# Performance work log

Measured on AMD Instinct MI355X. Metric: run time of the kernel, lower is better.

Reference implementation:

```python
import jax, jax.numpy as jnp
import numpy as np

B, L, D, H = 4, 1024, 1024, 16
HD = D // H            # head_dim = 64
MAX_LEN = 1024         # pos_max_len
SCALE = HD ** 0.5


def setup_inputs() -> dict:
    key = jax.random.key(0)
    ks = jax.random.split(key, 7)
    sd = 1.0 / np.sqrt(D)
    x = jax.random.normal(ks[0], (B, L, D), dtype=jnp.float32)
    Wq = jax.random.normal(ks[1], (D, D), dtype=jnp.float32) * sd
    Wk = jax.random.normal(ks[2], (D, D), dtype=jnp.float32) * sd
    Wv = jax.random.normal(ks[3], (D, D), dtype=jnp.float32) * sd
    Wo = jax.random.normal(ks[4], (D, D), dtype=jnp.float32) * sd
    # relative positional embedding tables [2*max_len+1, head_dim]
    pek = jax.random.normal(ks[5], (2 * MAX_LEN + 1, HD), dtype=jnp.float32) / np.sqrt(HD)
    pev = jax.random.normal(ks[6], (2 * MAX_LEN + 1, HD), dtype=jnp.float32) / np.sqrt(HD)
    return {"x": x, "Wq": Wq, "Wk": Wk, "Wv": Wv, "Wo": Wo, "pek": pek, "pev": pev}


def _rel_idx(seq_len):
    r = jnp.arange(seq_len)
    dist = r[None, :] - r[:, None]                 # k - q, [L, L]
    return jnp.clip(dist, -MAX_LEN, MAX_LEN) + MAX_LEN


def reference(x, Wq, Wk, Wv, Wo, pek, pev):
    b, s, _ = x.shape
    # projections (nn.Linear: x @ W.T), split heads -> [b, h, s, d]
    def proj(W):
        return (x @ W.T).reshape(b, s, H, HD).transpose(0, 2, 1, 3)
    Q, K, V = proj(Wq), proj(Wk), proj(Wv)

    scores = jnp.einsum('bhqd,bhkd->bhqk', Q, K) / SCALE
    idx = _rel_idx(s)                              # [s, s]
    rel_k = pek[idx]                               # [s, s, hd]
    scores = scores + jnp.einsum('bhqd,qkd->bhqk', Q, rel_k) / SCALE

    causal = jnp.tril(jnp.ones((s, s), dtype=bool))
    scores = jnp.where(causal[None, None], scores, -jnp.inf)
    attn = jax.nn.softmax(scores, axis=-1)         # [b, h, q, k]

    out = jnp.einsum('bhqk,bhkd->bhqd', attn, V)
    rel_v = pev[idx]                               # [s, s, hd]
    out = out + jnp.einsum('bhqk,qkd->bhqd', attn, rel_v)

    out = out.transpose(0, 2, 1, 3).reshape(b, s, D)
    return out @ Wo.T
```

## Files before the change

### kernel.cpp

```cpp
#include <hip/hip_runtime.h>
#include <hip/hip_bf16.h>

typedef __hip_bfloat16 bf16;
using bfv8 = __attribute__((ext_vector_type(8))) __bf16;
using f4_t = __attribute__((ext_vector_type(4))) float;

#define DEVI static __device__ __forceinline__

DEVI unsigned short f2bu(float f) {
    bf16 h = __float2bfloat16(f);
    return __builtin_bit_cast(unsigned short, h);
}
DEVI ushort4 f4_to_b4(float4 v) {
    ushort4 r;
    r.x = f2bu(v.x); r.y = f2bu(v.y); r.z = f2bu(v.z); r.w = f2bu(v.w);
    return r;
}
DEVI void gl2lds16(const void* g, void* l) {
    __builtin_amdgcn_global_load_lds((const __attribute__((address_space(1))) void*)g,
                                     (__attribute__((address_space(3))) void*)l, 16, 0, 0);
}

template<int N>
DEVI float row_ror(float x) {
    return __builtin_bit_cast(float,
        __builtin_amdgcn_update_dpp(0, __builtin_bit_cast(int, x), 0x120 | N, 0xF, 0xF, false));
}
DEVI float max16(float x) {
    x = fmaxf(x, row_ror<8>(x));
    x = fmaxf(x, row_ror<4>(x));
    x = fmaxf(x, row_ror<2>(x));
    x = fmaxf(x, row_ror<1>(x));
    return x;
}
DEVI float sum16(float x) {
    x += row_ror<8>(x);
    x += row_ror<4>(x);
    x += row_ror<2>(x);
    x += row_ror<1>(x);
    return x;
}

__global__ __launch_bounds__(256) void prep_cast(
    const float* __restrict__ x, const float* __restrict__ wq, const float* __restrict__ wk,
    const float* __restrict__ wv, const float* __restrict__ wo,
    bf16* __restrict__ xb, bf16* __restrict__ wqb, bf16* __restrict__ wkb,
    bf16* __restrict__ wvb, bf16* __restrict__ wob)
{
    size_t i = (size_t)blockIdx.x * 256 + threadIdx.x;
    const size_t X4 = 1u << 20, W4 = 1u << 18;
    const float* src; bf16* dst; size_t off;
    if (i < X4)              { src = x;  dst = xb;  off = i; }
    else if (i < X4 + W4)    { src = wq; dst = wqb; off = i - X4; }
    else if (i < X4 + 2*W4)  { src = wk; dst = wkb; off = i - X4 - W4; }
    else if (i < X4 + 3*W4)  { src = wv; dst = wvb; off = i - X4 - 2*W4; }
    else                     { src = wo; dst = wob; off = i - X4 - 3*W4; }
    float4 v = ((const float4*)src)[off];
    ((ushort4*)dst)[off] = f4_to_b4(v);
}

__global__ __launch_bounds__(256) void prep_blocks(
    const float* __restrict__ pek, const float* __restrict__ pev,
    bf16* __restrict__ pekBlk, bf16* __restrict__ pevBlk)
{
    __shared__ bf16 t[64][72];
    const int b = blockIdx.x;
    const int r = threadIdx.x >> 2, c0 = (threadIdx.x & 3) * 16;

    if (b < 17) {
        const float* src = pek + (size_t)(64 * b + 1 + r) * 64 + c0;
        bf16* dst = pekBlk + (size_t)b * 4096 + r * 64 + c0;
#pragma unroll
        for (int j = 0; j < 16; j += 4)
            *(ushort4*)(dst + j) = f4_to_b4(*(const float4*)(src + j));
    }
    {
        const float* src = pev + (size_t)(64 * b + 1 + r) * 64 + c0;
#pragma unroll
        for (int j = 0; j < 16; j++) t[r][c0 + j] = __float2bfloat16(src[j]);
        __syncthreads();
        bf16* dst = pevBlk + (size_t)b * 4096 + r * 64 + c0;
#pragma unroll
        for (int j = 0; j < 16; j++) dst[j] = t[c0 + j][r];
    }
}

__global__ __launch_bounds__(256) void transpose_v(const bf16* __restrict__ Vb, bf16* __restrict__ Vtb)
{
    __shared__ __align__(16) bf16 t[64][72];
    const int bh = blockIdx.y, l0 = blockIdx.x * 64;
    const int r = threadIdx.x >> 2, c0 = (threadIdx.x & 3) * 16;
    const bf16* src = Vb + ((size_t)(bh << 10) + l0 + r) * 64 + c0;
    *(int4*)&t[r][c0]     = *(const int4*)src;
    *(int4*)&t[r][c0 + 8] = *(const int4*)(src + 8);
    __syncthreads();
    int4 o[2]; bf16* ob = (bf16*)o;
#pragma unroll
    for (int j = 0; j < 16; j++) ob[j] = t[c0 + j][r];
    bf16* dst = Vtb + ((size_t)(bh << 6) + r) * 1024 + l0 + c0;
    *(int4*)dst = o[0]; *(int4*)(dst + 8) = o[1];
}

__global__ __launch_bounds__(256) void gemm_bt2(
    const bf16* __restrict__ A,
    const bf16* __restrict__ B0, const bf16* __restrict__ B1, const bf16* __restrict__ B2,
    bf16* __restrict__ outb, float* __restrict__ outf, int K, int mode)
{
    __shared__ __align__(16) bf16 As[128 * 64];
    __shared__ __align__(16) bf16 Bs[128 * 64];

    const int tid  = threadIdx.x;
    const int lane = tid & 63, wave = tid >> 6;
    const int quad = lane >> 4, l16 = lane & 15;
    const int wr = wave >> 1, wc = wave & 1;
    const int m0 = blockIdx.y * 128, n0 = blockIdx.x * 128;
    const int z = blockIdx.z;
    const bf16* Bm = (z == 0) ? B0 : (z == 1) ? B1 : B2;

    f4_t zero = {0.f, 0.f, 0.f, 0.f};
    f4_t acc[4][4];
#pragma unroll
    for (int i = 0; i < 4; i++)
#pragma unroll
        for (int j = 0; j < 4; j++) acc[i][j] = zero;

    const int srow = 32 * wave + (lane >> 3);
    const int scol = (lane & 7) * 8;
    const bf16* Ag = A  + (size_t)(m0 + srow) * K + scol;
    const bf16* Bg = Bm + (size_t)(n0 + srow) * K + scol;

    for (int k0 = 0; k0 < K; k0 += 64) {
#pragma unroll
        for (int i = 0; i < 4; i++) {
            gl2lds16(Ag + (size_t)(8 * i) * K + k0, &As[(32 * wave + 8 * i) * 64]);
            gl2lds16(Bg + (size_t)(8 * i) * K + k0, &Bs[(32 * wave + 8 * i) * 64]);
        }
        __syncthreads();
#pragma unroll
        for (int ks = 0; ks < 2; ks++) {
            bfv8 af[4], bfr[4];
#pragma unroll
            for (int mt = 0; mt < 4; mt++)
                af[mt] = *(const bfv8*)&As[(wr * 64 + mt * 16 + l16) * 64 + ks * 32 + quad * 8];
#pragma unroll
            for (int nt = 0; nt < 4; nt++)
                bfr[nt] = *(const bfv8*)&Bs[(wc * 64 + nt * 16 + l16) * 64 + ks * 32 + quad * 8];
#pragma unroll
            for (int mt = 0; mt < 4; mt++)
#pragma unroll
                for (int nt = 0; nt < 4; nt++)
                    acc[mt][nt] = __builtin_amdgcn_mfma_f32_16x16x32_bf16(af[mt], bfr[nt], acc[mt][nt], 0, 0, 0);
        }
        __syncthreads();
    }

    if (mode == 0) {
        bf16* ob = outb + (size_t)z * (4 * 16 * 1024 * 64);
#pragma unroll
        for (int mt = 0; mt < 4; mt++)
#pragma unroll
            for (int nt = 0; nt < 4; nt++)
#pragma unroll
                for (int r = 0; r < 4; r++) {
                    int m = m0 + wr * 64 + mt * 16 + quad * 4 + r;
                    int n = n0 + wc * 64 + nt * 16 + l16;
                    int b = m >> 10, l = m & 1023, h = n >> 6, hd = n & 63;
                    ob[((size_t)(b * 16 + h) * 1024 + l) * 64 + hd] = __float2bfloat16(acc[mt][nt][r]);
                }
    } else {
#pragma unroll
        for (int mt = 0; mt < 4; mt++)
#pragma unroll
            for (int nt = 0; nt < 4; nt++)
#pragma unroll
                for (int r = 0; r < 4; r++) {
                    int m = m0 + wr * 64 + mt * 16 + quad * 4 + r;
                    int n = n0 + wc * 64 + nt * 16 + l16;
                    outf[(size_t)m * 1024 + n] = acc[mt][nt][r];
                }
    }
}

__global__ __launch_bounds__(256) void attn_k(
    const bf16* __restrict__ Qb, const bf16* __restrict__ Kb, const bf16* __restrict__ Vtb,
    const bf16* __restrict__ pekBlk, const bf16* __restrict__ pevBlk, bf16* __restrict__ Ob)
{
    constexpr int ST = 104;
    __shared__ __align__(16) bf16 Ks[64 * 64];
    __shared__ __align__(16) bf16 Vs[64 * 64];
    __shared__ __align__(16) bf16 pekR[2 * 4096];
    __shared__ __align__(16) bf16 pevR[3 * 4096];
    __shared__ __align__(16) bf16 sU[4][16 * ST];
    __shared__ __align__(16) bf16 sP[4][16 * 72];

    const int tid  = threadIdx.x;
    const int lane = tid & 63, wave = tid >> 6;
    const int quad = lane >> 4, l16 = lane & 15;
    const int bh = blockIdx.x;
    const int g  = 15 - blockIdx.y;
    const int s  = 4 * g + wave;
    const int nkt = g + 1;

    bf16* myU = sU[wave];
    bf16* myP = sP[wave];

    const int srow8 = lane >> 3;
    const int scg   = (lane & 7) ^ srow8;
    const int x8    = l16 & 7;

    {
        int* p = (int*)myU;
#pragma unroll
        for (int i = 0; i < 13; i++) p[lane + 64 * i] = 0;
    }

    bfv8 qf[2];
    {
        const bf16* qp = Qb + ((size_t)bh * 1024 + 16 * s + l16) * 64 + quad * 8;
        qf[0] = *(const bfv8*)qp;
        qf[1] = *(const bfv8*)(qp + 32);
#pragma unroll
        for (int j = 0; j < 8; j++) {
            qf[0][j] = (__bf16)((float)qf[0][j] * 0.125f);
            qf[1][j] = (__bf16)((float)qf[1][j] * 0.125f);
        }
    }

    f4_t zero = {0.f, 0.f, 0.f, 0.f};
    f4_t o_acc[4];
    float m_i[4], l_i[4];
#pragma unroll
    for (int i = 0; i < 4; i++) { o_acc[i] = zero; m_i[i] = -1e30f; l_i[i] = 0.f; }

    const bf16* Kbh = Kb  + (size_t)bh * 1024 * 64;
    const bf16* Vbh = Vtb + (size_t)bh * 64 * 1024;
    const int B0 = 15 - g;

#pragma unroll
    for (int i = 0; i < 2; i++) {
        const int row = 8 * wave + 32 * i + srow8;
        gl2lds16(Kbh + (size_t)row * 64 + scg * 8, &Ks[(8 * wave + 32 * i) * 64]);
        gl2lds16(Vbh + (size_t)row * 1024 + scg * 8, &Vs[(8 * wave + 32 * i) * 64]);
    }
#pragma unroll
    for (int i2 = 0; i2 < 2; i2++) {
        const int slot = (B0 + i2) & 1;
#pragma unroll
        for (int i = 0; i < 2; i++) {
            const int row = 16 * wave + 8 * i + srow8;
            gl2lds16(pekBlk + (size_t)(B0 + i2) * 4096 + row * 64 + scg * 8,
                     &pekR[slot * 4096 + (16 * wave + 8 * i) * 64]);
        }
    }
#pragma unroll
    for (int i2 = 0; i2 < 3; i2++) {
        const int slot = (B0 + i2) % 3;
#pragma unroll
        for (int i = 0; i < 2; i++) {
            const int row = 16 * wave + 8 * i + srow8;
            gl2lds16(pevBlk + (size_t)(B0 + i2) * 4096 + row * 64 + scg * 8,
                     &pevR[slot * 4096 + (16 * wave + 8 * i) * 64]);
        }
    }

    for (int kt = 0; kt < nkt; kt++) {
        const int k0 = kt << 6;
        const int Bb = kt - g + 15;
        const int bm3 = Bb % 3;

        if (kt > 0) {
#pragma unroll
            for (int i = 0; i < 2; i++) {
                const int row = 8 * wave + 32 * i + srow8;
                gl2lds16(Kbh + (size_t)(k0 + row) * 64 + scg * 8, &Ks[(8 * wave + 32 * i) * 64]);
                gl2lds16(Vbh + (size_t)row * 1024 + k0 + scg * 8, &Vs[(8 * wave + 32 * i) * 64]);
            }
            const int bNew = Bb + 1, cNew = Bb + 2;
            const int slotK = bNew & 1, slotV = cNew % 3;
#pragma unroll
            for (int i = 0; i < 2; i++) {
                const int row = 16 * wave + 8 * i + srow8;
                gl2lds16(pekBlk + (size_t)bNew * 4096 + row * 64 + scg * 8,
                         &pekR[slotK * 4096 + (16 * wave + 8 * i) * 64]);
                gl2lds16(pevBlk + (size_t)cNew * 4096 + row * 64 + scg * 8,
                         &pevR[slotV * 4096 + (16 * wave + 8 * i) * 64]);
            }
        }
        __syncthreads();

        f4_t s1[4], tt[5];
#pragma unroll
        for (int i = 0; i < 4; i++) s1[i] = zero;
#pragma unroll
        for (int i = 0; i < 5; i++) tt[i] = zero;
#pragma unroll
        for (int ks = 0; ks < 2; ks++) {
#pragma unroll
            for (int nt = 0; nt < 4; nt++) {
                bfv8 kf = *(const bfv8*)&Ks[(nt * 16 + l16) * 64 + ((ks * 4 + quad) ^ x8) * 8];
                s1[nt] = __builtin_amdgcn_mfma_f32_16x16x32_bf16(qf[ks], kf, s1[nt], 0, 0, 0);
            }
#pragma unroll
            for (int nt = 0; nt < 5; nt++) {
                const int off  = 48 - 16 * wave + 16 * nt;
                const int slot = (Bb + (off >> 6)) & 1;
                bfv8 pf = *(const bfv8*)&pekR[slot * 4096 + ((off & 63) + l16) * 64
                                              + ((ks * 4 + quad) ^ x8) * 8];
                tt[nt] = __builtin_amdgcn_mfma_f32_16x16x32_bf16(qf[ks], pf, tt[nt], 0, 0, 0);
            }
        }

        float sc[4][4];
#pragma unroll
        for (int r = 0; r < 4; r++) {
            int qq = quad * 4 + r;
            int t  = l16 + 15 - qq;
            int srcl = quad * 16 + (t & 15);
            bool lo = (t < 16);
            float rot[5];
#pragma unroll
            for (int j = 0; j < 5; j++) rot[j] = __shfl(tt[j][r], srcl, 64);
#pragma unroll
            for (int nt = 0; nt < 4; nt++) {
                float s2 = lo ? rot[nt] : rot[nt + 1];
                float v = s1[nt][r] + s2;
                int kk = nt * 16 + l16;
                if (k0 + kk > 16 * s + qq) v = -1e30f;
                sc[nt][r] = v;
            }
        }

        float alpha[4];
#pragma unroll
        for (int r = 0; r < 4; r++) {
            float mt = fmaxf(fmaxf(sc[0][r], sc[1][r]), fmaxf(sc[2][r], sc[3][r]));
            mt = max16(mt);
            float mnew = fmaxf(m_i[r], mt);
            alpha[r] = __expf(m_i[r] - mnew);
            m_i[r] = mnew;
        }
#pragma unroll
        for (int nt = 0; nt < 4; nt++)
#pragma unroll
            for (int r = 0; r < 4; r++)
                sc[nt][r] = __expf(sc[nt][r] - m_i[r]);
#pragma unroll
        for (int r = 0; r < 4; r++) {
            float rs = sum16(sc[0][r] + sc[1][r] + sc[2][r] + sc[3][r]);
            l_i[r] = l_i[r] * alpha[r] + rs;
#pragma unroll
            for (int nt = 0; nt < 4; nt++) o_acc[nt][r] *= alpha[r];
        }

#pragma unroll
        for (int nt = 0; nt < 4; nt++)
#pragma unroll
            for (int r = 0; r < 4; r++) {
                int qq = quad * 4 + r;
                int kk = nt * 16 + l16;
                bf16 pb = __float2bfloat16(sc[nt][r]);
                myP[qq * 72 + kk] = pb;
                myU[qq * ST + kk - qq + 15] = pb;
            }

#pragma unroll
        for (int ks = 0; ks < 2; ks++) {
            bfv8 pa = *(const bfv8*)&myP[l16 * 72 + ks * 32 + quad * 8];
#pragma unroll
            for (int nt = 0; nt < 4; nt++) {
                bfv8 vf = *(const bfv8*)&Vs[(nt * 16 + l16) * 64 + ((ks * 4 + quad) ^ x8) * 8];
                o_acc[nt] = __builtin_amdgcn_mfma_f32_16x16x32_bf16(pa, vf, o_acc[nt], 0, 0, 0);
            }
        }
#pragma unroll
        for (int ks = 0; ks < 3; ks++) {
            bfv8 ua = *(const bfv8*)&myU[l16 * ST + ks * 32 + quad * 8];
            const int off2 = 48 - 16 * wave + 32 * ks + 8 * quad;
            int slot2 = bm3 + (off2 >> 6);
            if (slot2 >= 3) slot2 -= 3;
            const int chunk = (((off2 & 63) >> 3) ^ x8);
#pragma unroll
            for (int nt = 0; nt < 4; nt++) {
                bfv8 pvf = *(const bfv8*)&pevR[slot2 * 4096 + (nt * 16 + l16) * 64 + chunk * 8];
                o_acc[nt] = __builtin_amdgcn_mfma_f32_16x16x32_bf16(ua, pvf, o_acc[nt], 0, 0, 0);
            }
        }
        __syncthreads();
    }

    const int b = bh >> 4, h = bh & 15;
#pragma unroll
    for (int nt = 0; nt < 4; nt++)
#pragma unroll
        for (int r = 0; r < 4; r++) {
            int q = 16 * s + quad * 4 + r;
            int d = nt * 16 + l16;
            Ob[((size_t)(b * 1024 + q)) * 1024 + h * 64 + d] = __float2bfloat16(o_acc[nt][r] / l_i[r]);
        }
}

extern "C" void kernel_launch(void* const* d_in, const int* in_sizes, int n_in,
                              void* d_out, int out_size, void* d_ws, size_t ws_size,
                              hipStream_t stream) {
    const float* x   = (const float*)d_in[0];
    const float* Wq  = (const float*)d_in[1];
    const float* Wk  = (const float*)d_in[2];
    const float* Wv  = (const float*)d_in[3];
    const float* Wo  = (const float*)d_in[4];
    const float* pek = (const float*)d_in[5];
    const float* pev = (const float*)d_in[6];

    const size_t MB = 1u << 20;
    char* ws = (char*)d_ws;
    bf16* xb     = (bf16*)(ws + 0);
    bf16* Wqb    = (bf16*)(ws + 8  * MB);
    bf16* Wkb    = (bf16*)(ws + 10 * MB);
    bf16* Wvb    = (bf16*)(ws + 12 * MB);
    bf16* Wob    = (bf16*)(ws + 14 * MB);
    bf16* Qb     = (bf16*)(ws + 16 * MB);
    bf16* Kb     = (bf16*)(ws + 24 * MB);
    bf16* Vb     = (bf16*)(ws + 32 * MB);
    bf16* Vtb    = (bf16*)(ws + 40 * MB);
    bf16* pekBlk = (bf16*)(ws + 48 * MB);
    bf16* pevBlk = (bf16*)(ws + 48 * MB + 256*1024);
    bf16* Ao     = xb;

    prep_cast<<<dim3(8192), 256, 0, stream>>>(x, Wq, Wk, Wv, Wo, xb, Wqb, Wkb, Wvb, Wob);
    prep_blocks<<<dim3(18), 256, 0, stream>>>(pek, pev, pekBlk, pevBlk);
    gemm_bt2<<<dim3(8, 32, 3), 256, 0, stream>>>(xb, Wqb, Wkb, Wvb, Qb, nullptr, 1024, 0);
    transpose_v<<<dim3(16, 64), 256, 0, stream>>>(Vb, Vtb);
    attn_k<<<dim3(64, 16), 256, 0, stream>>>(Qb, Kb, Vtb, pekBlk, pevBlk, Ao);
    gemm_bt2<<<dim3(8, 32, 1), 256, 0, stream>>>(Ao, Wob, nullptr, nullptr, nullptr, (float*)d_out, 1024, 1);
}
```

Measured before the change: 247.8 us.

## Register-prefetch next tiles in GEMM and attention, halve GEMM M-tile

Both the projection GEMM and the attention kernel now load the next K/V/pek/pev or A/B tile into registers before computing the current tile, then write it to LDS after a barrier. This hides global load latency behind MFMA work, where the old code issued async global-to-LDS loads and waited on them right away. The GEMM tile shrinks from 128x128 to 64x128 and the grid doubles, giving more blocks to fill the CUs. The cost is more registers, extra LDS store instructions, and the loss of the direct global-to-LDS path.

```diff
diff --git a/kernel.cpp b/kernel.cpp
--- a/kernel.cpp
+++ b/kernel.cpp
@@ -106,75 +106,91 @@
     const bf16* __restrict__ B0, const bf16* __restrict__ B1, const bf16* __restrict__ B2,
     bf16* __restrict__ outb, float* __restrict__ outf, int K, int mode)
 {
-    __shared__ __align__(16) bf16 As[128 * 64];
+    __shared__ __align__(16) bf16 As[64 * 64];
     __shared__ __align__(16) bf16 Bs[128 * 64];
 
     const int tid  = threadIdx.x;
     const int lane = tid & 63, wave = tid >> 6;
     const int quad = lane >> 4, l16 = lane & 15;
     const int wr = wave >> 1, wc = wave & 1;
-    const int m0 = blockIdx.y * 128, n0 = blockIdx.x * 128;
+    const int m0 = blockIdx.y * 64, n0 = blockIdx.x * 128;
     const int z = blockIdx.z;
     const bf16* Bm = (z == 0) ? B0 : (z == 1) ? B1 : B2;
 
     f4_t zero = {0.f, 0.f, 0.f, 0.f};
-    f4_t acc[4][4];
+    f4_t acc[2][4];
+#pragma unroll
+    for (int i = 0; i < 2; i++)
+#pragma unroll
+        for (int j = 0; j < 4; j++) acc[i][j] = zero;
+
+    const int srow8 = lane >> 3;
+    const int scol  = (lane & 7) * 8;
+    const bf16* Ag = A  + (size_t)(m0 + 16 * wave + srow8) * K + scol;
+    const bf16* Bg = Bm + (size_t)(n0 + 32 * wave + srow8) * K + scol;
+
+#pragma unroll
+    for (int i = 0; i < 2; i++)
+        gl2lds16(Ag + (size_t)(8 * i) * K, &As[(16 * wave + 8 * i) * 64]);
 #pragma unroll
     for (int i = 0; i < 4; i++)
-#pragma unroll
-        for (int j = 0; j < 4; j++) acc[i][j] = zero;
-
-    const int srow = 32 * wave + (lane >> 3);
-    const int scol = (lane & 7) * 8;
-    const bf16* Ag = A  + (size_t)(m0 + srow) * K + scol;
-    const bf16* Bg = Bm + (size_t)(n0 + srow) * K + scol;
-
-    for (int k0 = 0; k0 < K; k0 += 64) {
-#pragma unroll
-        for (int i = 0; i < 4; i++) {
-            gl2lds16(Ag + (size_t)(8 * i) * K + k0, &As[(32 * wave + 8 * i) * 64]);
-            gl2lds16(Bg + (size_t)(8 * i) * K + k0, &Bs[(32 * wave + 8 * i) * 64]);
-        }
+        gl2lds16(Bg + (size_t)(8 * i) * K, &Bs[(32 * wave + 8 * i) * 64]);
+
+    for (int k0 = 0;;) {
         __syncthreads();
+        const bool more = (k0 + 64 < K);
+        int4 pa[2], pb[4];
+        if (more) {
+#pragma unroll
+            for (int i = 0; i < 2; i++) pa[i] = *(const int4*)(Ag + (size_t)(8 * i) * K + k0 + 64);
+#pragma unroll
+            for (int i = 0; i < 4; i++) pb[i] = *(const int4*)(Bg + (size_t)(8 * i) * K + k0 + 64);
+        }
 #pragma unroll
         for (int ks = 0; ks < 2; ks++) {
-            bfv8 af[4], bfr[4];
-#pragma unroll
-            for (int mt = 0; mt < 4; mt++)
-                af[mt] = *(const bfv8*)&As[(wr * 64 + mt * 16 + l16) * 64 + ks * 32 + quad * 8];
+            bfv8 af[2], bfr[4];
+#pragma unroll
+            for (int mt = 0; mt < 2; mt++)
+                af[mt] = *(const bfv8*)&As[(wr * 32 + mt * 16 + l16) * 64 + ks * 32 + quad * 8];
 #pragma unroll
             for (int nt = 0; nt < 4; nt++)
                 bfr[nt] = *(const bfv8*)&Bs[(wc * 64 + nt * 16 + l16) * 64 + ks * 32 + quad * 8];
 #pragma unroll
-            for (int mt = 0; mt < 4; mt++)
+            for (int mt = 0; mt < 2; mt++)
 #pragma unroll
                 for (int nt = 0; nt < 4; nt++)
                     acc[mt][nt] = __builtin_amdgcn_mfma_f32_16x16x32_bf16(af[mt], bfr[nt], acc[mt][nt], 0, 0, 0);
         }
+        if (!more) break;
         __syncthreads();
+#pragma unroll
+        for (int i = 0; i < 2; i++) *(int4*)&As[(16 * wave + 8 * i) * 64 + lane * 8] = pa[i];
+#pragma unroll
+        for (int i = 0; i < 4; i++) *(int4*)&Bs[(32 * wave + 8 * i) * 64 + lane * 8] = pb[i];
+        k0 += 64;
     }
 
     if (mode == 0) {
         bf16* ob = outb + (size_t)z * (4 * 16 * 1024 * 64);
 #pragma unroll
-        for (int mt = 0; mt < 4; mt++)
+        for (int mt = 0; mt < 2; mt++)
 #pragma unroll
             for (int nt = 0; nt < 4; nt++)
 #pragma unroll
                 for (int r = 0; r < 4; r++) {
-                    int m = m0 + wr * 64 + mt * 16 + quad * 4 + r;
+                    int m = m0 + wr * 32 + mt * 16 + quad * 4 + r;
                     int n = n0 + wc * 64 + nt * 16 + l16;
                     int b = m >> 10, l = m & 1023, h = n >> 6, hd = n & 63;
                     ob[((size_t)(b * 16 + h) * 1024 + l) * 64 + hd] = __float2bfloat16(acc[mt][nt][r]);
                 }
     } else {
 #pragma unroll
-        for (int mt = 0; mt < 4; mt++)
+        for (int mt = 0; mt < 2; mt++)
 #pragma unroll
             for (int nt = 0; nt < 4; nt++)
 #pragma unroll
                 for (int r = 0; r < 4; r++) {
-                    int m = m0 + wr * 64 + mt * 16 + quad * 4 + r;
+                    int m = m0 + wr * 32 + mt * 16 + quad * 4 + r;
                     int n = n0 + wc * 64 + nt * 16 + l16;
                     outf[(size_t)m * 1024 + n] = acc[mt][nt][r];
                 }
@@ -262,31 +278,31 @@
                      &pevR[slot * 4096 + (16 * wave + 8 * i) * 64]);
         }
     }
+    __syncthreads();
 
     for (int kt = 0; kt < nkt; kt++) {
         const int k0 = kt << 6;
         const int Bb = kt - g + 15;
         const int bm3 = Bb % 3;
-
-        if (kt > 0) {
-#pragma unroll
-            for (int i = 0; i < 2; i++) {
-                const int row = 8 * wave + 32 * i + srow8;
-                gl2lds16(Kbh + (size_t)(k0 + row) * 64 + scg * 8, &Ks[(8 * wave + 32 * i) * 64]);
-                gl2lds16(Vbh + (size_t)row * 1024 + k0 + scg * 8, &Vs[(8 * wave + 32 * i) * 64]);
-            }
-            const int bNew = Bb + 1, cNew = Bb + 2;
-            const int slotK = bNew & 1, slotV = cNew % 3;
-#pragma unroll
-            for (int i = 0; i < 2; i++) {
-                const int row = 16 * wave + 8 * i + srow8;
-                gl2lds16(pekBlk + (size_t)bNew * 4096 + row * 64 + scg * 8,
-                         &pekR[slotK * 4096 + (16 * wave + 8 * i) * 64]);
-                gl2lds16(pevBlk + (size_t)cNew * 4096 + row * 64 + scg * 8,
-                         &pevR[slotV * 4096 + (16 * wave + 8 * i) * 64]);
-            }
-        }
-        __syncthreads();
+        const bool hasNext = (kt + 1 < nkt);
+        const int ktn = hasNext ? kt + 1 : kt;
+        const int k0n = ktn << 6;
+        const int bN  = ktn - g + 16;
+        const int cN  = ktn - g + 17;
+
+        int4 pK0, pK1, pV0, pV1, pE0, pE1, pX0, pX1;
+        {
+            const int rowA = 8 * wave + srow8;
+            pK0 = *(const int4*)(Kbh + (size_t)(k0n + rowA) * 64 + scg * 8);
+            pK1 = *(const int4*)(Kbh + (size_t)(k0n + rowA + 32) * 64 + scg * 8);
+            pV0 = *(const int4*)(Vbh + (size_t)rowA * 1024 + k0n + scg * 8);
+            pV1 = *(const int4*)(Vbh + (size_t)(rowA + 32) * 1024 + k0n + scg * 8);
+            const int row16 = 16 * wave + srow8;
+            pE0 = *(const int4*)(pekBlk + (size_t)bN * 4096 + row16 * 64 + scg * 8);
+            pE1 = *(const int4*)(pekBlk + (size_t)bN * 4096 + (row16 + 8) * 64 + scg * 8);
+            pX0 = *(const int4*)(pevBlk + (size_t)cN * 4096 + row16 * 64 + scg * 8);
+            pX1 = *(const int4*)(pevBlk + (size_t)cN * 4096 + (row16 + 8) * 64 + scg * 8);
+        }
 
         f4_t s1[4], tt[5];
 #pragma unroll
@@ -385,7 +401,20 @@
                 o_acc[nt] = __builtin_amdgcn_mfma_f32_16x16x32_bf16(ua, pvf, o_acc[nt], 0, 0, 0);
             }
         }
+
         __syncthreads();
+        if (hasNext) {
+            *(int4*)&Ks[(8 * wave) * 64 + lane * 8]        = pK0;
+            *(int4*)&Ks[(8 * wave + 32) * 64 + lane * 8]   = pK1;
+            *(int4*)&Vs[(8 * wave) * 64 + lane * 8]        = pV0;
+            *(int4*)&Vs[(8 * wave + 32) * 64 + lane * 8]   = pV1;
+            const int sK = bN & 1, sV = cN % 3;
+            *(int4*)&pekR[sK * 4096 + (16 * wave) * 64 + lane * 8]     = pE0;
+            *(int4*)&pekR[sK * 4096 + (16 * wave + 8) * 64 + lane * 8] = pE1;
+            *(int4*)&pevR[sV * 4096 + (16 * wave) * 64 + lane * 8]     = pX0;
+            *(int4*)&pevR[sV * 4096 + (16 * wave + 8) * 64 + lane * 8] = pX1;
+            __syncthreads();
+        }
     }
 
     const int b = bh >> 4, h = bh & 15;
@@ -427,8 +456,8 @@
 
     prep_cast<<<dim3(8192), 256, 0, stream>>>(x, Wq, Wk, Wv, Wo, xb, Wqb, Wkb, Wvb, Wob);
     prep_blocks<<<dim3(18), 256, 0, stream>>>(pek, pev, pekBlk, pevBlk);
-    gemm_bt2<<<dim3(8, 32, 3), 256, 0, stream>>>(xb, Wqb, Wkb, Wvb, Qb, nullptr, 1024, 0);
+    gemm_bt2<<<dim3(8, 64, 3), 256, 0, stream>>>(xb, Wqb, Wkb, Wvb, Qb, nullptr, 1024, 0);
     transpose_v<<<dim3(16, 64), 256, 0, stream>>>(Vb, Vtb);
     attn_k<<<dim3(64, 16), 256, 0, stream>>>(Qb, Kb, Vtb, pekBlk, pevBlk, Ao);
-    gemm_bt2<<<dim3(8, 32, 1), 256, 0, stream>>>(Ao, Wob, nullptr, nullptr, nullptr, (float*)d_out, 1024, 1);
-}
+    gemm_bt2<<<dim3(8, 64, 1), 256, 0, stream>>>(Ao, Wob, nullptr, nullptr, nullptr, (float*)d_out, 1024, 1);
+}
```

After: 375.0 us. 51.3% more time.

## Prefetch next K/V/pos tiles into registers to overlap with compute

Applied to the files above, without the earlier changes.

Replaces the direct global-to-LDS async loads issued at the top of each key tile with register prefetches of the next tile's K, V, pek and pev blocks. These are issued before the current tile's MFMA work and written to LDS after a barrier at the end of the iteration. The aim is to hide global memory latency behind the compute instead of waiting on it before each tile. The cost is higher register pressure from eight int4 prefetch registers, an extra barrier per iteration, and a risk that the reused LDS slot indexing (swizzle, slot rotation) no longer matches the previous layout.

```diff
diff --git a/kernel.cpp b/kernel.cpp
--- a/kernel.cpp
+++ b/kernel.cpp
@@ -262,31 +262,31 @@
                      &pevR[slot * 4096 + (16 * wave + 8 * i) * 64]);
         }
     }
+    __syncthreads();
 
     for (int kt = 0; kt < nkt; kt++) {
         const int k0 = kt << 6;
         const int Bb = kt - g + 15;
         const int bm3 = Bb % 3;
-
-        if (kt > 0) {
-#pragma unroll
-            for (int i = 0; i < 2; i++) {
-                const int row = 8 * wave + 32 * i + srow8;
-                gl2lds16(Kbh + (size_t)(k0 + row) * 64 + scg * 8, &Ks[(8 * wave + 32 * i) * 64]);
-                gl2lds16(Vbh + (size_t)row * 1024 + k0 + scg * 8, &Vs[(8 * wave + 32 * i) * 64]);
-            }
-            const int bNew = Bb + 1, cNew = Bb + 2;
-            const int slotK = bNew & 1, slotV = cNew % 3;
-#pragma unroll
-            for (int i = 0; i < 2; i++) {
-                const int row = 16 * wave + 8 * i + srow8;
-                gl2lds16(pekBlk + (size_t)bNew * 4096 + row * 64 + scg * 8,
-                         &pekR[slotK * 4096 + (16 * wave + 8 * i) * 64]);
-                gl2lds16(pevBlk + (size_t)cNew * 4096 + row * 64 + scg * 8,
-                         &pevR[slotV * 4096 + (16 * wave + 8 * i) * 64]);
-            }
-        }
-        __syncthreads();
+        const bool hasNext = (kt + 1 < nkt);
+        const int ktn = hasNext ? kt + 1 : kt;
+        const int k0n = ktn << 6;
+        const int bN  = ktn - g + 16;
+        const int cN  = ktn - g + 17;
+
+        int4 pK0, pK1, pV0, pV1, pE0, pE1, pX0, pX1;
+        {
+            const int rowA = 8 * wave + srow8;
+            pK0 = *(const int4*)(Kbh + (size_t)(k0n + rowA) * 64 + scg * 8);
+            pK1 = *(const int4*)(Kbh + (size_t)(k0n + rowA + 32) * 64 + scg * 8);
+            pV0 = *(const int4*)(Vbh + (size_t)rowA * 1024 + k0n + scg * 8);
+            pV1 = *(const int4*)(Vbh + (size_t)(rowA + 32) * 1024 + k0n + scg * 8);
+            const int row16 = 16 * wave + srow8;
+            pE0 = *(const int4*)(pekBlk + (size_t)bN * 4096 + row16 * 64 + scg * 8);
+            pE1 = *(const int4*)(pekBlk + (size_t)bN * 4096 + (row16 + 8) * 64 + scg * 8);
+            pX0 = *(const int4*)(pevBlk + (size_t)cN * 4096 + row16 * 64 + scg * 8);
+            pX1 = *(const int4*)(pevBlk + (size_t)cN * 4096 + (row16 + 8) * 64 + scg * 8);
+        }
 
         f4_t s1[4], tt[5];
 #pragma unroll
@@ -385,7 +385,20 @@
                 o_acc[nt] = __builtin_amdgcn_mfma_f32_16x16x32_bf16(ua, pvf, o_acc[nt], 0, 0, 0);
             }
         }
+
         __syncthreads();
+        if (hasNext) {
+            *(int4*)&Ks[(8 * wave) * 64 + lane * 8]        = pK0;
+            *(int4*)&Ks[(8 * wave + 32) * 64 + lane * 8]   = pK1;
+            *(int4*)&Vs[(8 * wave) * 64 + lane * 8]        = pV0;
+            *(int4*)&Vs[(8 * wave + 32) * 64 + lane * 8]   = pV1;
+            const int sK = bN & 1, sV = cN % 3;
+            *(int4*)&pekR[sK * 4096 + (16 * wave) * 64 + lane * 8]     = pE0;
+            *(int4*)&pekR[sK * 4096 + (16 * wave + 8) * 64 + lane * 8] = pE1;
+            *(int4*)&pevR[sV * 4096 + (16 * wave) * 64 + lane * 8]     = pX0;
+            *(int4*)&pevR[sV * 4096 + (16 * wave + 8) * 64 + lane * 8] = pX1;
+            __syncthreads();
+        }
     }
 
     const int b = bh >> 4, h = bh & 15;
```

After: 243.7 us. Within noise of the previous version (-1.7%).

## Fuse V transpose into QKV GEMM epilogue and shrink GEMM tile to 64x128

Applied to the files above, without the earlier changes.

Removes the separate transpose_v kernel by having the QKV GEMM write V directly in transposed layout through an LDS-staged epilogue. Q and K outputs are also staged through LDS so the head-split stores become coalesced 16-byte writes instead of scattered 2-byte stores. The M tile is halved to 64 rows, doubling the grid, with launch bounds asking for 4 blocks per CU. The trade is less operand reuse per block in exchange for more parallelism, plus an extra LDS round-trip in the epilogue.

```diff
diff --git a/kernel.cpp b/kernel.cpp
--- a/kernel.cpp
+++ b/kernel.cpp
@@ -85,68 +85,56 @@
     }
 }
 
-__global__ __launch_bounds__(256) void transpose_v(const bf16* __restrict__ Vb, bf16* __restrict__ Vtb)
-{
-    __shared__ __align__(16) bf16 t[64][72];
-    const int bh = blockIdx.y, l0 = blockIdx.x * 64;
-    const int r = threadIdx.x >> 2, c0 = (threadIdx.x & 3) * 16;
-    const bf16* src = Vb + ((size_t)(bh << 10) + l0 + r) * 64 + c0;
-    *(int4*)&t[r][c0]     = *(const int4*)src;
-    *(int4*)&t[r][c0 + 8] = *(const int4*)(src + 8);
-    __syncthreads();
-    int4 o[2]; bf16* ob = (bf16*)o;
-#pragma unroll
-    for (int j = 0; j < 16; j++) ob[j] = t[c0 + j][r];
-    bf16* dst = Vtb + ((size_t)(bh << 6) + r) * 1024 + l0 + c0;
-    *(int4*)dst = o[0]; *(int4*)(dst + 8) = o[1];
-}
-
-__global__ __launch_bounds__(256) void gemm_bt2(
+__global__ __launch_bounds__(256, 4) void gemm_bt3(
     const bf16* __restrict__ A,
     const bf16* __restrict__ B0, const bf16* __restrict__ B1, const bf16* __restrict__ B2,
-    bf16* __restrict__ outb, float* __restrict__ outf, int K, int mode)
+    bf16* __restrict__ outb, bf16* __restrict__ vtb, float* __restrict__ outf,
+    int K, int mode)
 {
-    __shared__ __align__(16) bf16 As[128 * 64];
-    __shared__ __align__(16) bf16 Bs[128 * 64];
+    __shared__ __align__(16) bf16 smem[64 * 64 + 128 * 64];
+    bf16* As = smem;
+    bf16* Bs = smem + 64 * 64;
+    bf16* Cb = smem;
 
     const int tid  = threadIdx.x;
     const int lane = tid & 63, wave = tid >> 6;
     const int quad = lane >> 4, l16 = lane & 15;
     const int wr = wave >> 1, wc = wave & 1;
-    const int m0 = blockIdx.y * 128, n0 = blockIdx.x * 128;
+    const int m0 = blockIdx.y * 64, n0 = blockIdx.x * 128;
     const int z = blockIdx.z;
     const bf16* Bm = (z == 0) ? B0 : (z == 1) ? B1 : B2;
 
     f4_t zero = {0.f, 0.f, 0.f, 0.f};
-    f4_t acc[4][4];
-#pragma unroll
-    for (int i = 0; i < 4; i++)
+    f4_t acc[2][4];
+#pragma unroll
+    for (int i = 0; i < 2; i++)
 #pragma unroll
         for (int j = 0; j < 4; j++) acc[i][j] = zero;
 
-    const int srow = 32 * wave + (lane >> 3);
-    const int scol = (lane & 7) * 8;
-    const bf16* Ag = A  + (size_t)(m0 + srow) * K + scol;
-    const bf16* Bg = Bm + (size_t)(n0 + srow) * K + scol;
+    const int srow8 = lane >> 3;
+    const int scol  = (lane & 7) * 8;
+    const bf16* Ag = A  + (size_t)(m0 + 16 * wave + srow8) * K + scol;
+    const bf16* Bg = Bm + (size_t)(n0 + 32 * wave + srow8) * K + scol;
 
     for (int k0 = 0; k0 < K; k0 += 64) {
 #pragma unroll
-        for (int i = 0; i < 4; i++) {
-            gl2lds16(Ag + (size_t)(8 * i) * K + k0, &As[(32 * wave + 8 * i) * 64]);
+        for (int i = 0; i < 2; i++)
+            gl2lds16(Ag + (size_t)(8 * i) * K + k0, &As[(16 * wave + 8 * i) * 64]);
+#pragma unroll
+        for (int i = 0; i < 4; i++)
             gl2lds16(Bg + (size_t)(8 * i) * K + k0, &Bs[(32 * wave + 8 * i) * 64]);
-        }
         __syncthreads();
 #pragma unroll
         for (int ks = 0; ks < 2; ks++) {
-            bfv8 af[4], bfr[4];
-#pragma unroll
-            for (int mt = 0; mt < 4; mt++)
-                af[mt] = *(const bfv8*)&As[(wr * 64 + mt * 16 + l16) * 64 + ks * 32 + quad * 8];
+            bfv8 af[2], bfr[4];
+#pragma unroll
+            for (int mt = 0; mt < 2; mt++)
+                af[mt] = *(const bfv8*)&As[(wr * 32 + mt * 16 + l16) * 64 + ks * 32 + quad * 8];
 #pragma unroll
             for (int nt = 0; nt < 4; nt++)
                 bfr[nt] = *(const bfv8*)&Bs[(wc * 64 + nt * 16 + l16) * 64 + ks * 32 + quad * 8];
 #pragma unroll
-            for (int mt = 0; mt < 4; mt++)
+            for (int mt = 0; mt < 2; mt++)
 #pragma unroll
                 for (int nt = 0; nt < 4; nt++)
                     acc[mt][nt] = __builtin_amdgcn_mfma_f32_16x16x32_bf16(af[mt], bfr[nt], acc[mt][nt], 0, 0, 0);
@@ -154,30 +142,59 @@
         __syncthreads();
     }
 
-    if (mode == 0) {
-        bf16* ob = outb + (size_t)z * (4 * 16 * 1024 * 64);
-#pragma unroll
-        for (int mt = 0; mt < 4; mt++)
+    if (mode == 1) {
+#pragma unroll
+        for (int mt = 0; mt < 2; mt++)
 #pragma unroll
             for (int nt = 0; nt < 4; nt++)
 #pragma unroll
                 for (int r = 0; r < 4; r++) {
-                    int m = m0 + wr * 64 + mt * 16 + quad * 4 + r;
-                    int n = n0 + wc * 64 + nt * 16 + l16;
-                    int b = m >> 10, l = m & 1023, h = n >> 6, hd = n & 63;
-                    ob[((size_t)(b * 16 + h) * 1024 + l) * 64 + hd] = __float2bfloat16(acc[mt][nt][r]);
-                }
-    } else {
-#pragma unroll
-        for (int mt = 0; mt < 4; mt++)
-#pragma unroll
-            for (int nt = 0; nt < 4; nt++)
-#pragma unroll
-                for (int r = 0; r < 4; r++) {
-                    int m = m0 + wr * 64 + mt * 16 + quad * 4 + r;
+                    int m = m0 + wr * 32 + mt * 16 + quad * 4 + r;
                     int n = n0 + wc * 64 + nt * 16 + l16;
                     outf[(size_t)m * 1024 + n] = acc[mt][nt][r];
                 }
+        return;
+    }
+
+    const int b  = m0 >> 10, l0 = m0 & 1023, h0 = n0 >> 6;
+    if (z < 2) {
+#pragma unroll
+        for (int mt = 0; mt < 2; mt++)
+#pragma unroll
+            for (int nt = 0; nt < 4; nt++)
+#pragma unroll
+                for (int r = 0; r < 4; r++) {
+                    int mm = wr * 32 + mt * 16 + quad * 4 + r;
+                    int nn = wc * 64 + nt * 16 + l16;
+                    Cb[mm * 136 + nn] = __float2bfloat16(acc[mt][nt][r]);
+                }
+        __syncthreads();
+        bf16* ob = outb + (size_t)z * (4 * 16 * 1024 * 64);
+        const int ri = tid >> 1, hp = ri >> 6, lrow = ri & 63, c0 = (tid & 1) * 32;
+        bf16* dst = ob + ((size_t)((b * 16 + h0 + hp) * 1024) + l0 + lrow) * 64 + c0;
+        const bf16* srcl = &Cb[lrow * 136 + hp * 64 + c0];
+#pragma unroll
+        for (int j = 0; j < 4; j++)
+            *(int4*)(dst + 8 * j) = *(const int4*)(srcl + 8 * j);
+    } else {
+#pragma unroll
+        for (int mt = 0; mt < 2; mt++)
+#pragma unroll
+            for (int nt = 0; nt < 4; nt++)
+#pragma unroll
+                for (int r = 0; r < 4; r++) {
+                    int mm = wr * 32 + mt * 16 + quad * 4 + r;
+                    int nn = wc * 64 + nt * 16 + l16;
+                    Cb[nn * 72 + mm] = __float2bfloat16(acc[mt][nt][r]);
+                }
+        __syncthreads();
+        const int ri = tid >> 1, c0 = (tid & 1) * 32;
+        const int n = n0 + ri, h = n >> 6, hd = n & 63;
+        bf16* dst = vtb + ((size_t)((b * 16 + h) * 64 + hd)) * 1024 + l0 + c0;
+        const bf16* srcl = &Cb[ri * 72 + c0];
+#pragma unroll
+        for (int j = 0; j < 4; j++)
+            *(int4*)(dst + 8 * j) = *(const int4*)(srcl + 8 * j);
     }
 }
 
@@ -419,16 +436,14 @@
     bf16* Wob    = (bf16*)(ws + 14 * MB);
     bf16* Qb     = (bf16*)(ws + 16 * MB);
     bf16* Kb     = (bf16*)(ws + 24 * MB);
-    bf16* Vb     = (bf16*)(ws + 32 * MB);
-    bf16* Vtb    = (bf16*)(ws + 40 * MB);
+    bf16* Vtb    = (bf16*)(ws + 32 * MB);
     bf16* pekBlk = (bf16*)(ws + 48 * MB);
     bf16* pevBlk = (bf16*)(ws + 48 * MB + 256*1024);
     bf16* Ao     = xb;
 
     prep_cast<<<dim3(8192), 256, 0, stream>>>(x, Wq, Wk, Wv, Wo, xb, Wqb, Wkb, Wvb, Wob);
     prep_blocks<<<dim3(18), 256, 0, stream>>>(pek, pev, pekBlk, pevBlk);
-    gemm_bt2<<<dim3(8, 32, 3), 256, 0, stream>>>(xb, Wqb, Wkb, Wvb, Qb, nullptr, 1024, 0);
-    transpose_v<<<dim3(16, 64), 256, 0, stream>>>(Vb, Vtb);
+    gemm_bt3<<<dim3(8, 64, 3), 256, 0, stream>>>(xb, Wqb, Wkb, Wvb, Qb, Vtb, nullptr, 1024, 0);
     attn_k<<<dim3(64, 16), 256, 0, stream>>>(Qb, Kb, Vtb, pekBlk, pevBlk, Ao);
-    gemm_bt2<<<dim3(8, 32, 1), 256, 0, stream>>>(Ao, Wob, nullptr, nullptr, nullptr, (float*)d_out, 1024, 1);
-}
+    gemm_bt3<<<dim3(8, 64, 1), 256, 0, stream>>>(Ao, Wob, nullptr, nullptr, nullptr, nullptr, (float*)d_out, 1024, 1);
+}
```

Measured after the change: 237.9 us. -4.0%, faster.
